# Optimization experiments

Measured on AMD Instinct MI355X. Metric: run time of the kernel, lower is better.

Reference implementation:

```python
import jax, jax.numpy as jnp
import numpy as np

N_ATOMS = 200000
N_EDGES = 800000
ATOM_FDIM = 133
HIDDEN = 256
NUM_MOLS = 8000
ALPHA = 0.2  # LeakyReLU slope


def setup_inputs() -> dict:
    key = jax.random.key(0)
    ks = jax.random.split(key, 10)
    f_atoms = jax.random.normal(ks[0], (N_ATOMS, ATOM_FDIM), dtype=jnp.float32)
    edge_index = jax.random.randint(ks[1], (2, N_EDGES), 0, N_ATOMS, dtype=jnp.int64)
    mol_ids = jnp.sort(jax.random.randint(ks[2], (N_ATOMS,), 0, NUM_MOLS, dtype=jnp.int64))
    s0 = 1.0 / np.sqrt(ATOM_FDIM)
    sh = 1.0 / np.sqrt(HIDDEN)
    sa = 1.0 / np.sqrt(2 * HIDDEN)
    W0 = jax.random.normal(ks[3], (ATOM_FDIM, HIDDEN), dtype=jnp.float32) * s0
    a0 = jax.random.normal(ks[4], (2 * HIDDEN,), dtype=jnp.float32) * sa
    W1 = jax.random.normal(ks[5], (HIDDEN, HIDDEN), dtype=jnp.float32) * sh
    a1 = jax.random.normal(ks[6], (2 * HIDDEN,), dtype=jnp.float32) * sa
    W2 = jax.random.normal(ks[7], (HIDDEN, HIDDEN), dtype=jnp.float32) * sh
    a2 = jax.random.normal(ks[8], (2 * HIDDEN,), dtype=jnp.float32) * sa
    return {"f_atoms": f_atoms, "edge_index": edge_index, "mol_ids": mol_ids,
            "W0": W0, "a0": a0, "W1": W1, "a1": a1, "W2": W2, "a2": a2}


def _gat_layer(x, W, a, src, tgt, residual):
    # x: [N, Fin], W: [Fin, H], a: [2H]
    h = x @ W                              # [N, H]
    H = h.shape[1]
    a_s, a_t = a[:H], a[H:]
    # e = leakyrelu([h_src || h_tgt] @ a), computed without materializing the concat
    e = jax.nn.leaky_relu(h[src] @ a_s + h[tgt] @ a_t, negative_slope=ALPHA)  # [E]
    att = jnp.exp(e)
    denom = jax.ops.segment_sum(att, tgt, num_segments=x.shape[0])            # [N]
    att_n = att / (denom[tgt] + 1e-8)
    # weighted scatter-aggregate (dropout is a no-op in eval mode)
    h_prime = jax.ops.segment_sum(h[src] * att_n[:, None], tgt, num_segments=x.shape[0])
    if residual:
        h_prime = h_prime + x
    return jax.nn.elu(h_prime)


def reference(f_atoms, edge_index, mol_ids, W0, a0, W1, a1, W2, a2):
    src, tgt = edge_index[0], edge_index[1]
    x = _gat_layer(f_atoms, W0, a0, src, tgt, residual=False)
    x = _gat_layer(x, W1, a1, src, tgt, residual=True)
    x = _gat_layer(x, W2, a2, src, tgt, residual=True)
    # per-molecule mean pooling (a_scope loop -> segment mean)
    sums = jax.ops.segment_sum(x, mol_ids, num_segments=NUM_MOLS)            # [M, H]
    counts = jax.ops.segment_sum(jnp.ones((x.shape[0],), x.dtype), mol_ids, num_segments=NUM_MOLS)
    return jnp.where(counts[:, None] > 0, sums / jnp.maximum(counts[:, None], 1.0), 0.0)
```

## Files before the change

### kernel.cpp

```cpp
#include <hip/hip_runtime.h>

#define N_ATOMS 200000
#define N_EDGES 800000
#define FDIM    133
#define HID     256
#define NMOLS   8000
#define CAP     32

typedef unsigned short bf16_t;
typedef __attribute__((ext_vector_type(4))) float f32x4;
typedef __attribute__((ext_vector_type(8))) short bf16x8;

__device__ inline float bf2f(bf16_t u) {
    union { unsigned int i; float f; } v; v.i = ((unsigned int)u) << 16; return v.f;
}
__device__ inline bf16_t f2bf(float f) {
    union { float f; unsigned int i; } v; v.f = f;
    return (bf16_t)((v.i + 0x7fffu + ((v.i >> 16) & 1u)) >> 16);
}
__device__ inline float4 ld4(const bf16_t* p) {
    ushort4 u = *(const ushort4*)p;
    return make_float4(bf2f(u.x), bf2f(u.y), bf2f(u.z), bf2f(u.w));
}
__device__ inline void st4(bf16_t* p, float4 v) {
    ushort4 u; u.x = f2bf(v.x); u.y = f2bf(v.y); u.z = f2bf(v.z); u.w = f2bf(v.w);
    *(ushort4*)p = u;
}

__device__ inline void gload_lds16(const void* g, void* l) {
    __builtin_amdgcn_global_load_lds((const __attribute__((address_space(1))) unsigned int*)g,
                                     (__attribute__((address_space(3))) unsigned int*)l,
                                     16, 0, 0);
}

__global__ __launch_bounds__(256) void build_adj(const int* __restrict__ ei,
                                                 int* __restrict__ cnt,
                                                 int* __restrict__ lst) {
    int e = blockIdx.x * 256 + threadIdx.x;
    if (e >= N_EDGES) return;
    int s = ei[e];
    int t = ei[N_EDGES + e];
    int p = atomicAdd(&cnt[t], 1);
    if (p < CAP) lst[t * CAP + p] = s;
}

__global__ __launch_bounds__(256) void transpose_w(const float* __restrict__ W,
                                                   bf16_t* __restrict__ Wt,
                                                   int K, int Kpad) {
    int idx = blockIdx.x * 256 + threadIdx.x;
    if (idx >= HID * Kpad) return;
    int n = idx / Kpad, k = idx - n * Kpad;
    Wt[idx] = (k < K) ? f2bf(W[k * HID + n]) : (bf16_t)0;
}

template <bool A_FP32, int KSTEPS, int LDA, int KP>
__global__ __launch_bounds__(512, 4) void gemm_mfma(const void* __restrict__ Av,
                                                    const bf16_t* __restrict__ Wt,
                                                    bf16_t* __restrict__ H,
                                                    const float* __restrict__ avec,
                                                    float* __restrict__ ssp,
                                                    float* __restrict__ stp) {
    __shared__ bf16_t As[128][32];
    __shared__ bf16_t Bs[256][32];
    const int tid  = threadIdx.x;
    const int lane = tid & 63;
    const int w    = tid >> 6;
    const int wr   = w >> 2;
    const int wc   = w & 3;
    const int fr   = lane & 15;
    const int kg   = lane >> 4;
    const int row0 = blockIdx.x * 128;

    const int sra  = tid >> 2;
    const int ska  = (tid & 3) * 8;
    int sgrow = row0 + sra; if (sgrow >= N_ATOMS) sgrow = N_ATOMS - 1;

    ssp += (long long)wc * N_ATOMS;
    stp += (long long)wc * N_ATOMS;

    f32x4 acc[4][4] = {};

    for (int ks = 0; ks < KSTEPS; ++ks) {
        const int k0 = ks * 32;
        if (ks) __syncthreads();

        if constexpr (A_FP32) {
            const float* A = (const float*)Av;
            short v[8];
            #pragma unroll
            for (int j = 0; j < 8; ++j) {
                int gk = k0 + ska + j;
                v[j] = (gk < LDA) ? (short)f2bf(A[(long long)sgrow * LDA + gk]) : (short)0;
            }
            *(bf16x8*)&As[sra][ska] = *(bf16x8*)v;
        } else {
            gload_lds16((const bf16_t*)Av + (long long)sgrow * LDA + k0 + ska,
                        (char*)&As[0][0] + w * 1024);
        }
        gload_lds16(Wt + (long long)(tid >> 2) * KP + k0 + ska,
                    (char*)&Bs[0][0] + w * 1024);
        gload_lds16(Wt + (long long)(128 + (tid >> 2)) * KP + k0 + ska,
                    (char*)&Bs[0][0] + 8192 + w * 1024);
        __syncthreads();

        const int koff = kg * 8;
        bf16x8 af[4], bfr[4];
        #pragma unroll
        for (int i = 0; i < 4; ++i)
            af[i] = *(const bf16x8*)&As[wr * 64 + i * 16 + fr][koff];
        #pragma unroll
        for (int jn = 0; jn < 4; ++jn)
            bfr[jn] = *(const bf16x8*)&Bs[wc * 64 + jn * 16 + fr][koff];
        #pragma unroll
        for (int i = 0; i < 4; ++i)
            #pragma unroll
            for (int jn = 0; jn < 4; ++jn)
                acc[i][jn] = __builtin_amdgcn_mfma_f32_16x16x32_bf16(af[i], bfr[jn], acc[i][jn], 0, 0, 0);
    }

    float as_v[4], at_v[4];
    #pragma unroll
    for (int jn = 0; jn < 4; ++jn) {
        int c = wc * 64 + jn * 16 + fr;
        as_v[jn] = avec[c];
        at_v[jn] = avec[HID + c];
    }
    #pragma unroll
    for (int i = 0; i < 4; ++i) {
        #pragma unroll
        for (int rr = 0; rr < 4; ++rr) {
            int r = row0 + wr * 64 + i * 16 + kg * 4 + rr;
            float ps = 0.f, pt = 0.f;
            #pragma unroll
            for (int jn = 0; jn < 4; ++jn) {
                float h = acc[i][jn][rr];
                ps += h * as_v[jn];
                pt += h * at_v[jn];
                if (r < N_ATOMS)
                    H[(long long)r * HID + (wc * 64 + jn * 16 + fr)] = f2bf(h);
            }
            #pragma unroll
            for (int o = 1; o < 16; o <<= 1) {
                ps += __shfl_xor(ps, o);
                pt += __shfl_xor(pt, o);
            }
            if (fr == 0 && r < N_ATOMS) {
                ssp[r] = ps;
                stp[r] = pt;
            }
        }
    }
}

__global__ __launch_bounds__(256) void combine_dots(const float* __restrict__ ssp,
                                                    const float* __restrict__ stp,
                                                    float* __restrict__ ss,
                                                    float* __restrict__ st) {
    int i = blockIdx.x * 256 + threadIdx.x;
    if (i >= N_ATOMS) return;
    ss[i] = (ssp[i] + ssp[N_ATOMS + i]) + (ssp[2 * N_ATOMS + i] + ssp[3 * N_ATOMS + i]);
    st[i] = (stp[i] + stp[N_ATOMS + i]) + (stp[2 * N_ATOMS + i] + stp[3 * N_ATOMS + i]);
}

__global__ __launch_bounds__(256) void aggregate(const bf16_t* __restrict__ H,
                                                 const float* __restrict__ ss,
                                                 const float* __restrict__ st,
                                                 const int* __restrict__ cnt,
                                                 const int* __restrict__ lst,
                                                 bf16_t* __restrict__ X,
                                                 int residual) {
    int wave = threadIdx.x >> 6;
    int lane = threadIdx.x & 63;
    int t = blockIdx.x * 4 + wave;
    if (t >= N_ATOMS) return;
    int n = cnt[t]; if (n > CAP) n = CAP;
    float stt = st[t];
    const int base = t * CAP;

    float ax = 0.f, ay = 0.f, az = 0.f, aw = 0.f;
    float denom = 0.f;

    for (int i0 = 0; i0 < n; i0 += 4) {
        int4 s4 = *(const int4*)&lst[base + i0];
        int s0 = (i0 + 0 < n) ? s4.x : t;
        int s1 = (i0 + 1 < n) ? s4.y : t;
        int s2 = (i0 + 2 < n) ? s4.z : t;
        int s3 = (i0 + 3 < n) ? s4.w : t;

        float v0 = ss[s0], v1 = ss[s1], v2 = ss[s2], v3 = ss[s3];

        float e0 = v0 + stt; e0 = e0 > 0.f ? e0 : 0.2f * e0;
        float e1 = v1 + stt; e1 = e1 > 0.f ? e1 : 0.2f * e1;
        float e2 = v2 + stt; e2 = e2 > 0.f ? e2 : 0.2f * e2;
        float e3 = v3 + stt; e3 = e3 > 0.f ? e3 : 0.2f * e3;

        float t0 = (i0 + 0 < n) ? __expf(e0) : 0.f;
        float t1 = (i0 + 1 < n) ? __expf(e1) : 0.f;
        float t2 = (i0 + 2 < n) ? __expf(e2) : 0.f;
        float t3 = (i0 + 3 < n) ? __expf(e3) : 0.f;

        float4 h0 = ld4(&H[(long long)s0 * HID + lane * 4]);
        float4 h1 = ld4(&H[(long long)s1 * HID + lane * 4]);
        float4 h2 = ld4(&H[(long long)s2 * HID + lane * 4]);
        float4 h3 = ld4(&H[(long long)s3 * HID + lane * 4]);

        denom += (t0 + t1) + (t2 + t3);
        ax += t0 * h0.x + t1 * h1.x + t2 * h2.x + t3 * h3.x;
        ay += t0 * h0.y + t1 * h1.y + t2 * h2.y + t3 * h3.y;
        az += t0 * h0.z + t1 * h1.z + t2 * h2.z + t3 * h3.z;
        aw += t0 * h0.w + t1 * h1.w + t2 * h2.w + t3 * h3.w;
    }

    float inv = 1.f / (denom + 1e-8f);
    float rx = ax * inv, ry = ay * inv, rz = az * inv, rw = aw * inv;
    if (residual) {
        float4 xv = ld4(&X[(long long)t * HID + lane * 4]);
        rx += xv.x; ry += xv.y; rz += xv.z; rw += xv.w;
    }
    rx = rx > 0.f ? rx : (__expf(rx) - 1.f);
    ry = ry > 0.f ? ry : (__expf(ry) - 1.f);
    rz = rz > 0.f ? rz : (__expf(rz) - 1.f);
    rw = rw > 0.f ? rw : (__expf(rw) - 1.f);
    st4(&X[(long long)t * HID + lane * 4], make_float4(rx, ry, rz, rw));
}

__device__ inline int lower_bound_i(const int* a, int n, int v) {
    int lo = 0, hi = n;
    while (lo < hi) { int mid = (lo + hi) >> 1; if (a[mid] < v) lo = mid + 1; else hi = mid; }
    return lo;
}

__global__ __launch_bounds__(64) void pool_kernel(const bf16_t* __restrict__ X,
                                                  const int* __restrict__ mol,
                                                  float* __restrict__ out) {
    int m = blockIdx.x;
    int lane = threadIdx.x;
    int lo = lower_bound_i(mol, N_ATOMS, m);
    int hi = lower_bound_i(mol, N_ATOMS, m + 1);
    float ax = 0.f, ay = 0.f, az = 0.f, aw = 0.f;
    for (int i = lo; i < hi; ++i) {
        float4 v = ld4(&X[(long long)i * HID + lane * 4]);
        ax += v.x; ay += v.y; az += v.z; aw += v.w;
    }
    float c = (float)(hi - lo);
    float4 r = make_float4(0.f, 0.f, 0.f, 0.f);
    if (c > 0.f) {
        float inv = 1.f / c;
        r = make_float4(ax * inv, ay * inv, az * inv, aw * inv);
    }
    *(float4*)&out[(long long)m * HID + lane * 4] = r;
}

extern "C" void kernel_launch(void* const* d_in, const int* in_sizes, int n_in,
                              void* d_out, int out_size, void* d_ws, size_t ws_size,
                              hipStream_t stream) {
    const float* f_atoms = (const float*)d_in[0];
    const int*   ei      = (const int*)d_in[1];
    const int*   mol     = (const int*)d_in[2];
    const float* W0      = (const float*)d_in[3];
    const float* a0      = (const float*)d_in[4];
    const float* W1      = (const float*)d_in[5];
    const float* a1      = (const float*)d_in[6];
    const float* W2      = (const float*)d_in[7];
    const float* a2      = (const float*)d_in[8];
    float* out = (float*)d_out;

    char* ws = (char*)d_ws;
    size_t off = 0;
    bf16_t* X  = (bf16_t*)(ws + off); off += (size_t)N_ATOMS * HID * 2;
    bf16_t* Hb = (bf16_t*)(ws + off); off += (size_t)N_ATOMS * HID * 2;
    float* ss  = (float*)(ws + off);  off += (size_t)N_ATOMS * 4;
    float* st  = (float*)(ws + off);  off += (size_t)N_ATOMS * 4;
    int* cnt   = (int*)(ws + off);    off += (size_t)N_ATOMS * 4;
    int* lst   = (int*)(ws + off);    off += (size_t)N_ATOMS * CAP * 4;
    if (ws_size < off) return;

    char* ob = (char*)d_out;
    bf16_t* Wt  = (bf16_t*)ob;
    float*  ssp = (float*)(ob + 131072);
    float*  stp = (float*)(ob + 131072 + 3200000);

    hipMemsetAsync(cnt, 0, (size_t)N_ATOMS * 4, stream);
    build_adj<<<(N_EDGES + 255) / 256, 256, 0, stream>>>(ei, cnt, lst);

    const int gemm_blocks = (N_ATOMS + 127) / 128;
    const int agg_blocks  = N_ATOMS / 4;
    const int cmb_blocks  = (N_ATOMS + 255) / 256;

    transpose_w<<<(HID * 160 + 255) / 256, 256, 0, stream>>>(W0, Wt, FDIM, 160);
    gemm_mfma<true, 5, FDIM, 160><<<gemm_blocks, 512, 0, stream>>>(f_atoms, Wt, Hb, a0, ssp, stp);
    combine_dots<<<cmb_blocks, 256, 0, stream>>>(ssp, stp, ss, st);
    aggregate<<<agg_blocks, 256, 0, stream>>>(Hb, ss, st, cnt, lst, X, 0);

    transpose_w<<<(HID * HID + 255) / 256, 256, 0, stream>>>(W1, Wt, HID, HID);
    gemm_mfma<false, 8, HID, HID><<<gemm_blocks, 512, 0, stream>>>(X, Wt, Hb, a1, ssp, stp);
    combine_dots<<<cmb_blocks, 256, 0, stream>>>(ssp, stp, ss, st);
    aggregate<<<agg_blocks, 256, 0, stream>>>(Hb, ss, st, cnt, lst, X, 1);

    transpose_w<<<(HID * HID + 255) / 256, 256, 0, stream>>>(W2, Wt, HID, HID);
    gemm_mfma<false, 8, HID, HID><<<gemm_blocks, 512, 0, stream>>>(X, Wt, Hb, a2, ssp, stp);
    combine_dots<<<cmb_blocks, 256, 0, stream>>>(ssp, stp, ss, st);
    aggregate<<<agg_blocks, 256, 0, stream>>>(Hb, ss, st, cnt, lst, X, 1);

    pool_kernel<<<NMOLS, 64, 0, stream>>>(X, mol, out);
}
```

Before: 602.4 us.

## Fuse dot-product reduction into GEMM and make aggregate a prefetching persistent kernel

The per-column-group attention dot partials are now reduced through shared memory inside the GEMM epilogue and written straight to ss/st, which removes the combine_dots kernel and its partial-sum buffers. The aggregate kernel becomes a grid-stride persistent kernel with 2048 blocks. Each wave prefetches the next node's count, first neighbour indices, target score and residual while it works on the current node. Neighbour loads are now predicated instead of reading a padded self index, which avoids needless gathers. The cost is an extra __syncthreads and shared memory in the GEMM, plus more register pressure in aggregate.

```diff
diff --git a/kernel.cpp b/kernel.cpp
--- a/kernel.cpp
+++ b/kernel.cpp
@@ -6,6 +6,7 @@
 #define HID     256
 #define NMOLS   8000
 #define CAP     32
+#define AGG_BLOCKS 2048
 
 typedef unsigned short bf16_t;
 typedef __attribute__((ext_vector_type(4))) float f32x4;
@@ -58,10 +59,11 @@
                                                     const bf16_t* __restrict__ Wt,
                                                     bf16_t* __restrict__ H,
                                                     const float* __restrict__ avec,
-                                                    float* __restrict__ ssp,
-                                                    float* __restrict__ stp) {
+                                                    float* __restrict__ ss_o,
+                                                    float* __restrict__ st_o) {
     __shared__ bf16_t As[128][32];
     __shared__ bf16_t Bs[256][32];
+    __shared__ float  red[2][128][4];
     const int tid  = threadIdx.x;
     const int lane = tid & 63;
     const int w    = tid >> 6;
@@ -74,9 +76,6 @@
     const int sra  = tid >> 2;
     const int ska  = (tid & 3) * 8;
     int sgrow = row0 + sra; if (sgrow >= N_ATOMS) sgrow = N_ATOMS - 1;
-
-    ssp += (long long)wc * N_ATOMS;
-    stp += (long long)wc * N_ATOMS;
 
     f32x4 acc[4][4] = {};
 
@@ -129,7 +128,8 @@
     for (int i = 0; i < 4; ++i) {
         #pragma unroll
         for (int rr = 0; rr < 4; ++rr) {
-            int r = row0 + wr * 64 + i * 16 + kg * 4 + rr;
+            int row_l = wr * 64 + i * 16 + kg * 4 + rr;
+            int r = row0 + row_l;
             float ps = 0.f, pt = 0.f;
             #pragma unroll
             for (int jn = 0; jn < 4; ++jn) {
@@ -144,22 +144,20 @@
                 ps += __shfl_xor(ps, o);
                 pt += __shfl_xor(pt, o);
             }
-            if (fr == 0 && r < N_ATOMS) {
-                ssp[r] = ps;
-                stp[r] = pt;
+            if (fr == 0) {
+                red[0][row_l][wc] = ps;
+                red[1][row_l][wc] = pt;
             }
         }
     }
-}
-
-__global__ __launch_bounds__(256) void combine_dots(const float* __restrict__ ssp,
-                                                    const float* __restrict__ stp,
-                                                    float* __restrict__ ss,
-                                                    float* __restrict__ st) {
-    int i = blockIdx.x * 256 + threadIdx.x;
-    if (i >= N_ATOMS) return;
-    ss[i] = (ssp[i] + ssp[N_ATOMS + i]) + (ssp[2 * N_ATOMS + i] + ssp[3 * N_ATOMS + i]);
-    st[i] = (stp[i] + stp[N_ATOMS + i]) + (stp[2 * N_ATOMS + i] + stp[3 * N_ATOMS + i]);
+    __syncthreads();
+    if (tid < 128) {
+        int r = row0 + tid;
+        if (r < N_ATOMS) {
+            ss_o[r] = (red[0][tid][0] + red[0][tid][1]) + (red[0][tid][2] + red[0][tid][3]);
+            st_o[r] = (red[1][tid][0] + red[1][tid][1]) + (red[1][tid][2] + red[1][tid][3]);
+        }
+    }
 }
 
 __global__ __launch_bounds__(256) void aggregate(const bf16_t* __restrict__ H,
@@ -169,59 +167,92 @@
                                                  const int* __restrict__ lst,
                                                  bf16_t* __restrict__ X,
                                                  int residual) {
-    int wave = threadIdx.x >> 6;
-    int lane = threadIdx.x & 63;
-    int t = blockIdx.x * 4 + wave;
-    if (t >= N_ATOMS) return;
-    int n = cnt[t]; if (n > CAP) n = CAP;
-    float stt = st[t];
-    const int base = t * CAP;
-
-    float ax = 0.f, ay = 0.f, az = 0.f, aw = 0.f;
-    float denom = 0.f;
-
-    for (int i0 = 0; i0 < n; i0 += 4) {
-        int4 s4 = *(const int4*)&lst[base + i0];
-        int s0 = (i0 + 0 < n) ? s4.x : t;
-        int s1 = (i0 + 1 < n) ? s4.y : t;
-        int s2 = (i0 + 2 < n) ? s4.z : t;
-        int s3 = (i0 + 3 < n) ? s4.w : t;
-
-        float v0 = ss[s0], v1 = ss[s1], v2 = ss[s2], v3 = ss[s3];
+    const int lane   = threadIdx.x & 63;
+    const int nwaves = AGG_BLOCKS * 4;
+    int t = (blockIdx.x * 256 + threadIdx.x) >> 6;
+
+    int    n_c  = cnt[t];
+    int4   a_c  = *(const int4*)&lst[t * CAP];
+    float  st_c = st[t];
+    float4 xv_c = make_float4(0.f, 0.f, 0.f, 0.f);
+    if (residual) xv_c = ld4(&X[(size_t)(t * HID) + lane * 4]);
+
+    for (;;) {
+        const int t_n = t + nwaves;
+        const bool more = (t_n < N_ATOMS);
+        int n_x = 0; int4 a_x = make_int4(0, 0, 0, 0);
+        float st_x = 0.f; float4 xv_x = make_float4(0.f, 0.f, 0.f, 0.f);
+        if (more) {
+            n_x  = cnt[t_n];
+            a_x  = *(const int4*)&lst[t_n * CAP];
+            st_x = st[t_n];
+            if (residual) xv_x = ld4(&X[(size_t)(t_n * HID) + lane * 4]);
+        }
+
+        const int n = n_c < CAP ? n_c : CAP;
+        const float stt = st_c;
+        const float4 z = make_float4(0.f, 0.f, 0.f, 0.f);
+
+        float v0 = 0.f, v1 = 0.f, v2 = 0.f, v3 = 0.f;
+        float4 h0 = z, h1 = z, h2 = z, h3 = z;
+        if (n > 0) { v0 = ss[a_c.x]; h0 = ld4(&H[(size_t)(a_c.x * HID) + lane * 4]); }
+        if (n > 1) { v1 = ss[a_c.y]; h1 = ld4(&H[(size_t)(a_c.y * HID) + lane * 4]); }
+        if (n > 2) { v2 = ss[a_c.z]; h2 = ld4(&H[(size_t)(a_c.z * HID) + lane * 4]); }
+        if (n > 3) { v3 = ss[a_c.w]; h3 = ld4(&H[(size_t)(a_c.w * HID) + lane * 4]); }
 
         float e0 = v0 + stt; e0 = e0 > 0.f ? e0 : 0.2f * e0;
         float e1 = v1 + stt; e1 = e1 > 0.f ? e1 : 0.2f * e1;
         float e2 = v2 + stt; e2 = e2 > 0.f ? e2 : 0.2f * e2;
         float e3 = v3 + stt; e3 = e3 > 0.f ? e3 : 0.2f * e3;
-
-        float t0 = (i0 + 0 < n) ? __expf(e0) : 0.f;
-        float t1 = (i0 + 1 < n) ? __expf(e1) : 0.f;
-        float t2 = (i0 + 2 < n) ? __expf(e2) : 0.f;
-        float t3 = (i0 + 3 < n) ? __expf(e3) : 0.f;
-
-        float4 h0 = ld4(&H[(long long)s0 * HID + lane * 4]);
-        float4 h1 = ld4(&H[(long long)s1 * HID + lane * 4]);
-        float4 h2 = ld4(&H[(long long)s2 * HID + lane * 4]);
-        float4 h3 = ld4(&H[(long long)s3 * HID + lane * 4]);
-
-        denom += (t0 + t1) + (t2 + t3);
-        ax += t0 * h0.x + t1 * h1.x + t2 * h2.x + t3 * h3.x;
-        ay += t0 * h0.y + t1 * h1.y + t2 * h2.y + t3 * h3.y;
-        az += t0 * h0.z + t1 * h1.z + t2 * h2.z + t3 * h3.z;
-        aw += t0 * h0.w + t1 * h1.w + t2 * h2.w + t3 * h3.w;
-    }
-
-    float inv = 1.f / (denom + 1e-8f);
-    float rx = ax * inv, ry = ay * inv, rz = az * inv, rw = aw * inv;
-    if (residual) {
-        float4 xv = ld4(&X[(long long)t * HID + lane * 4]);
-        rx += xv.x; ry += xv.y; rz += xv.z; rw += xv.w;
-    }
-    rx = rx > 0.f ? rx : (__expf(rx) - 1.f);
-    ry = ry > 0.f ? ry : (__expf(ry) - 1.f);
-    rz = rz > 0.f ? rz : (__expf(rz) - 1.f);
-    rw = rw > 0.f ? rw : (__expf(rw) - 1.f);
-    st4(&X[(long long)t * HID + lane * 4], make_float4(rx, ry, rz, rw));
+        float w0 = (n > 0) ? __expf(e0) : 0.f;
+        float w1 = (n > 1) ? __expf(e1) : 0.f;
+        float w2 = (n > 2) ? __expf(e2) : 0.f;
+        float w3 = (n > 3) ? __expf(e3) : 0.f;
+
+        float denom = (w0 + w1) + (w2 + w3);
+        float ax = w0 * h0.x + w1 * h1.x + w2 * h2.x + w3 * h3.x;
+        float ay = w0 * h0.y + w1 * h1.y + w2 * h2.y + w3 * h3.y;
+        float az = w0 * h0.z + w1 * h1.z + w2 * h2.z + w3 * h3.z;
+        float aw = w0 * h0.w + w1 * h1.w + w2 * h2.w + w3 * h3.w;
+
+        for (int i0 = 4; i0 < n; i0 += 4) {
+            int4 s4 = *(const int4*)&lst[t * CAP + i0];
+            float vA = ss[s4.x];
+            float4 hA = ld4(&H[(size_t)(s4.x * HID) + lane * 4]);
+            float vB = 0.f, vC = 0.f, vD = 0.f;
+            float4 hB = z, hC = z, hD = z;
+            if (i0 + 1 < n) { vB = ss[s4.y]; hB = ld4(&H[(size_t)(s4.y * HID) + lane * 4]); }
+            if (i0 + 2 < n) { vC = ss[s4.z]; hC = ld4(&H[(size_t)(s4.z * HID) + lane * 4]); }
+            if (i0 + 3 < n) { vD = ss[s4.w]; hD = ld4(&H[(size_t)(s4.w * HID) + lane * 4]); }
+
+            float eA = vA + stt; eA = eA > 0.f ? eA : 0.2f * eA;
+            float eB = vB + stt; eB = eB > 0.f ? eB : 0.2f * eB;
+            float eC = vC + stt; eC = eC > 0.f ? eC : 0.2f * eC;
+            float eD = vD + stt; eD = eD > 0.f ? eD : 0.2f * eD;
+            float wA = __expf(eA);
+            float wB = (i0 + 1 < n) ? __expf(eB) : 0.f;
+            float wC = (i0 + 2 < n) ? __expf(eC) : 0.f;
+            float wD = (i0 + 3 < n) ? __expf(eD) : 0.f;
+
+            denom += (wA + wB) + (wC + wD);
+            ax += wA * hA.x + wB * hB.x + wC * hC.x + wD * hD.x;
+            ay += wA * hA.y + wB * hB.y + wC * hC.y + wD * hD.y;
+            az += wA * hA.z + wB * hB.z + wC * hC.z + wD * hD.z;
+            aw += wA * hA.w + wB * hB.w + wC * hC.w + wD * hD.w;
+        }
+
+        float inv = 1.f / (denom + 1e-8f);
+        float rx = ax * inv, ry = ay * inv, rz = az * inv, rw = aw * inv;
+        if (residual) { rx += xv_c.x; ry += xv_c.y; rz += xv_c.z; rw += xv_c.w; }
+        rx = rx > 0.f ? rx : (__expf(rx) - 1.f);
+        ry = ry > 0.f ? ry : (__expf(ry) - 1.f);
+        rz = rz > 0.f ? rz : (__expf(rz) - 1.f);
+        rw = rw > 0.f ? rw : (__expf(rw) - 1.f);
+        st4(&X[(size_t)(t * HID) + lane * 4], make_float4(rx, ry, rz, rw));
+
+        if (!more) break;
+        t = t_n; n_c = n_x; a_c = a_x; st_c = st_x; xv_c = xv_x;
+    }
 }
 
 __device__ inline int lower_bound_i(const int* a, int n, int v) {
@@ -275,32 +306,24 @@
     int* lst   = (int*)(ws + off);    off += (size_t)N_ATOMS * CAP * 4;
     if (ws_size < off) return;
 
-    char* ob = (char*)d_out;
-    bf16_t* Wt  = (bf16_t*)ob;
-    float*  ssp = (float*)(ob + 131072);
-    float*  stp = (float*)(ob + 131072 + 3200000);
+    bf16_t* Wt = (bf16_t*)d_out;
 
     hipMemsetAsync(cnt, 0, (size_t)N_ATOMS * 4, stream);
     build_adj<<<(N_EDGES + 255) / 256, 256, 0, stream>>>(ei, cnt, lst);
 
     const int gemm_blocks = (N_ATOMS + 127) / 128;
-    const int agg_blocks  = N_ATOMS / 4;
-    const int cmb_blocks  = (N_ATOMS + 255) / 256;
 
     transpose_w<<<(HID * 160 + 255) / 256, 256, 0, stream>>>(W0, Wt, FDIM, 160);
-    gemm_mfma<true, 5, FDIM, 160><<<gemm_blocks, 512, 0, stream>>>(f_atoms, Wt, Hb, a0, ssp, stp);
-    combine_dots<<<cmb_blocks, 256, 0, stream>>>(ssp, stp, ss, st);
-    aggregate<<<agg_blocks, 256, 0, stream>>>(Hb, ss, st, cnt, lst, X, 0);
+    gemm_mfma<true, 5, FDIM, 160><<<gemm_blocks, 512, 0, stream>>>(f_atoms, Wt, Hb, a0, ss, st);
+    aggregate<<<AGG_BLOCKS, 256, 0, stream>>>(Hb, ss, st, cnt, lst, X, 0);
 
     transpose_w<<<(HID * HID + 255) / 256, 256, 0, stream>>>(W1, Wt, HID, HID);
-    gemm_mfma<false, 8, HID, HID><<<gemm_blocks, 512, 0, stream>>>(X, Wt, Hb, a1, ssp, stp);
-    combine_dots<<<cmb_blocks, 256, 0, stream>>>(ssp, stp, ss, st);
-    aggregate<<<agg_blocks, 256, 0, stream>>>(Hb, ss, st, cnt, lst, X, 1);
+    gemm_mfma<false, 8, HID, HID><<<gemm_blocks, 512, 0, stream>>>(X, Wt, Hb, a1, ss, st);
+    aggregate<<<AGG_BLOCKS, 256, 0, stream>>>(Hb, ss, st, cnt, lst, X, 1);
 
     transpose_w<<<(HID * HID + 255) / 256, 256, 0, stream>>>(W2, Wt, HID, HID);
-    gemm_mfma<false, 8, HID, HID><<<gemm_blocks, 512, 0, stream>>>(X, Wt, Hb, a2, ssp, stp);
-    combine_dots<<<cmb_blocks, 256, 0, stream>>>(ssp, stp, ss, st);
-    aggregate<<<agg_blocks, 256, 0, stream>>>(Hb, ss, st, cnt, lst, X, 1);
+    gemm_mfma<false, 8, HID, HID><<<gemm_blocks, 512, 0, stream>>>(X, Wt, Hb, a2, ss, st);
+    aggregate<<<AGG_BLOCKS, 256, 0, stream>>>(Hb, ss, st, cnt, lst, X, 1);
 
     pool_kernel<<<NMOLS, 64, 0, stream>>>(X, mol, out);
 }
```

Result: no change. 601.6 us (-0.1%).

## Double-buffer GEMM LDS tiles and fuse attention-dot reduction into GEMM epilogue

Applied to the files above, without the earlier changes.

The GEMM now keeps two LDS buffers and issues the loads for the next K step before running the MFMAs on the current one, so global loads overlap with compute and one barrier per step is removed. The per-column-wave partial attention dots are now reduced in shared memory inside the GEMM epilogue. This removes the separate combine_dots kernel and the round trip of the partial sums through global memory. In exchange, LDS use per block roughly doubles, which may lower occupancy under the launch bounds of 4 blocks, and there is one extra block-wide sync at the end.

```diff
diff --git a/kernel.cpp b/kernel.cpp
--- a/kernel.cpp
+++ b/kernel.cpp
@@ -58,10 +58,11 @@
                                                     const bf16_t* __restrict__ Wt,
                                                     bf16_t* __restrict__ H,
                                                     const float* __restrict__ avec,
-                                                    float* __restrict__ ssp,
-                                                    float* __restrict__ stp) {
-    __shared__ bf16_t As[128][32];
-    __shared__ bf16_t Bs[256][32];
+                                                    float* __restrict__ ss_o,
+                                                    float* __restrict__ st_o) {
+    __shared__ bf16_t As[2][128][32];
+    __shared__ bf16_t Bs[2][256][32];
+    __shared__ float  red[2][128][4];
     const int tid  = threadIdx.x;
     const int lane = tid & 63;
     const int w    = tid >> 6;
@@ -75,48 +76,65 @@
     const int ska  = (tid & 3) * 8;
     int sgrow = row0 + sra; if (sgrow >= N_ATOMS) sgrow = N_ATOMS - 1;
 
-    ssp += (long long)wc * N_ATOMS;
-    stp += (long long)wc * N_ATOMS;
+    float sreg[8];
+
+#define ISSUE(ks_, buf_) do {                                                          \
+    const int k0_ = (ks_) * 32;                                                        \
+    if constexpr (A_FP32) {                                                            \
+        _Pragma("unroll")                                                              \
+        for (int j = 0; j < 8; ++j) {                                                  \
+            int gk = k0_ + ska + j;                                                    \
+            sreg[j] = (gk < LDA) ? ((const float*)Av)[(long long)sgrow * LDA + gk] : 0.f; \
+        }                                                                              \
+    } else {                                                                           \
+        gload_lds16((const bf16_t*)Av + (long long)sgrow * LDA + k0_ + ska,            \
+                    (char*)&As[buf_][0][0] + w * 1024);                                \
+    }                                                                                  \
+    gload_lds16(Wt + (long long)(tid >> 2) * KP + k0_ + ska,                           \
+                (char*)&Bs[buf_][0][0] + w * 1024);                                    \
+    gload_lds16(Wt + (long long)(128 + (tid >> 2)) * KP + k0_ + ska,                   \
+                (char*)&Bs[buf_][0][0] + 8192 + w * 1024);                             \
+} while (0)
+
+#define COMMIT(buf_) do {                                                              \
+    if constexpr (A_FP32) {                                                            \
+        short v_[8];                                                                   \
+        _Pragma("unroll")                                                              \
+        for (int j = 0; j < 8; ++j) v_[j] = (short)f2bf(sreg[j]);                      \
+        *(bf16x8*)&As[buf_][sra][ska] = *(bf16x8*)&v_[0];                              \
+    }                                                                                  \
+} while (0)
 
     f32x4 acc[4][4] = {};
 
+    ISSUE(0, 0);
+    COMMIT(0);
+    __syncthreads();
+
+    int buf = 0;
     for (int ks = 0; ks < KSTEPS; ++ks) {
-        const int k0 = ks * 32;
-        if (ks) __syncthreads();
-
-        if constexpr (A_FP32) {
-            const float* A = (const float*)Av;
-            short v[8];
-            #pragma unroll
-            for (int j = 0; j < 8; ++j) {
-                int gk = k0 + ska + j;
-                v[j] = (gk < LDA) ? (short)f2bf(A[(long long)sgrow * LDA + gk]) : (short)0;
-            }
-            *(bf16x8*)&As[sra][ska] = *(bf16x8*)v;
-        } else {
-            gload_lds16((const bf16_t*)Av + (long long)sgrow * LDA + k0 + ska,
-                        (char*)&As[0][0] + w * 1024);
-        }
-        gload_lds16(Wt + (long long)(tid >> 2) * KP + k0 + ska,
-                    (char*)&Bs[0][0] + w * 1024);
-        gload_lds16(Wt + (long long)(128 + (tid >> 2)) * KP + k0 + ska,
-                    (char*)&Bs[0][0] + 8192 + w * 1024);
-        __syncthreads();
+        if (ks + 1 < KSTEPS) ISSUE(ks + 1, buf ^ 1);
 
         const int koff = kg * 8;
         bf16x8 af[4], bfr[4];
         #pragma unroll
         for (int i = 0; i < 4; ++i)
-            af[i] = *(const bf16x8*)&As[wr * 64 + i * 16 + fr][koff];
+            af[i] = *(const bf16x8*)&As[buf][wr * 64 + i * 16 + fr][koff];
         #pragma unroll
         for (int jn = 0; jn < 4; ++jn)
-            bfr[jn] = *(const bf16x8*)&Bs[wc * 64 + jn * 16 + fr][koff];
+            bfr[jn] = *(const bf16x8*)&Bs[buf][wc * 64 + jn * 16 + fr][koff];
         #pragma unroll
         for (int i = 0; i < 4; ++i)
             #pragma unroll
             for (int jn = 0; jn < 4; ++jn)
                 acc[i][jn] = __builtin_amdgcn_mfma_f32_16x16x32_bf16(af[i], bfr[jn], acc[i][jn], 0, 0, 0);
-    }
+
+        if (ks + 1 < KSTEPS) COMMIT(buf ^ 1);
+        __syncthreads();
+        buf ^= 1;
+    }
+#undef ISSUE
+#undef COMMIT
 
     float as_v[4], at_v[4];
     #pragma unroll
@@ -129,7 +147,8 @@
     for (int i = 0; i < 4; ++i) {
         #pragma unroll
         for (int rr = 0; rr < 4; ++rr) {
-            int r = row0 + wr * 64 + i * 16 + kg * 4 + rr;
+            int row_l = wr * 64 + i * 16 + kg * 4 + rr;
+            int r = row0 + row_l;
             float ps = 0.f, pt = 0.f;
             #pragma unroll
             for (int jn = 0; jn < 4; ++jn) {
@@ -144,22 +163,20 @@
                 ps += __shfl_xor(ps, o);
                 pt += __shfl_xor(pt, o);
             }
-            if (fr == 0 && r < N_ATOMS) {
-                ssp[r] = ps;
-                stp[r] = pt;
+            if (fr == 0) {
+                red[0][row_l][wc] = ps;
+                red[1][row_l][wc] = pt;
             }
         }
     }
-}
-
-__global__ __launch_bounds__(256) void combine_dots(const float* __restrict__ ssp,
-                                                    const float* __restrict__ stp,
-                                                    float* __restrict__ ss,
-                                                    float* __restrict__ st) {
-    int i = blockIdx.x * 256 + threadIdx.x;
-    if (i >= N_ATOMS) return;
-    ss[i] = (ssp[i] + ssp[N_ATOMS + i]) + (ssp[2 * N_ATOMS + i] + ssp[3 * N_ATOMS + i]);
-    st[i] = (stp[i] + stp[N_ATOMS + i]) + (stp[2 * N_ATOMS + i] + stp[3 * N_ATOMS + i]);
+    __syncthreads();
+    if (tid < 128) {
+        int r = row0 + tid;
+        if (r < N_ATOMS) {
+            ss_o[r] = (red[0][tid][0] + red[0][tid][1]) + (red[0][tid][2] + red[0][tid][3]);
+            st_o[r] = (red[1][tid][0] + red[1][tid][1]) + (red[1][tid][2] + red[1][tid][3]);
+        }
+    }
 }
 
 __global__ __launch_bounds__(256) void aggregate(const bf16_t* __restrict__ H,
@@ -275,31 +292,24 @@
     int* lst   = (int*)(ws + off);    off += (size_t)N_ATOMS * CAP * 4;
     if (ws_size < off) return;
 
-    char* ob = (char*)d_out;
-    bf16_t* Wt  = (bf16_t*)ob;
-    float*  ssp = (float*)(ob + 131072);
-    float*  stp = (float*)(ob + 131072 + 3200000);
+    bf16_t* Wt = (bf16_t*)d_out;
 
     hipMemsetAsync(cnt, 0, (size_t)N_ATOMS * 4, stream);
     build_adj<<<(N_EDGES + 255) / 256, 256, 0, stream>>>(ei, cnt, lst);
 
     const int gemm_blocks = (N_ATOMS + 127) / 128;
     const int agg_blocks  = N_ATOMS / 4;
-    const int cmb_blocks  = (N_ATOMS + 255) / 256;
 
     transpose_w<<<(HID * 160 + 255) / 256, 256, 0, stream>>>(W0, Wt, FDIM, 160);
-    gemm_mfma<true, 5, FDIM, 160><<<gemm_blocks, 512, 0, stream>>>(f_atoms, Wt, Hb, a0, ssp, stp);
-    combine_dots<<<cmb_blocks, 256, 0, stream>>>(ssp, stp, ss, st);
+    gemm_mfma<true, 5, FDIM, 160><<<gemm_blocks, 512, 0, stream>>>(f_atoms, Wt, Hb, a0, ss, st);
     aggregate<<<agg_blocks, 256, 0, stream>>>(Hb, ss, st, cnt, lst, X, 0);
 
     transpose_w<<<(HID * HID + 255) / 256, 256, 0, stream>>>(W1, Wt, HID, HID);
-    gemm_mfma<false, 8, HID, HID><<<gemm_blocks, 512, 0, stream>>>(X, Wt, Hb, a1, ssp, stp);
-    combine_dots<<<cmb_blocks, 256, 0, stream>>>(ssp, stp, ss, st);
+    gemm_mfma<false, 8, HID, HID><<<gemm_blocks, 512, 0, stream>>>(X, Wt, Hb, a1, ss, st);
     aggregate<<<agg_blocks, 256, 0, stream>>>(Hb, ss, st, cnt, lst, X, 1);
 
     transpose_w<<<(HID * HID + 255) / 256, 256, 0, stream>>>(W2, Wt, HID, HID);
-    gemm_mfma<false, 8, HID, HID><<<gemm_blocks, 512, 0, stream>>>(X, Wt, Hb, a2, ssp, stp);
-    combine_dots<<<cmb_blocks, 256, 0, stream>>>(ssp, stp, ss, st);
+    gemm_mfma<false, 8, HID, HID><<<gemm_blocks, 512, 0, stream>>>(X, Wt, Hb, a2, ss, st);
     aggregate<<<agg_blocks, 256, 0, stream>>>(Hb, ss, st, cnt, lst, X, 1);
 
     pool_kernel<<<NMOLS, 64, 0, stream>>>(X, mol, out);
```

Result: faster. 582.3 us (-3.3%).
